# Optimization experiments

Hardware: AMD Instinct MI355X
Metric: run time of the kernel (lower is better)

## Reference

```python
import jax, jax.numpy as jnp
import numpy as np
from jax import lax

DN = ('NCDHW', 'OIDHW', 'NCDHW')
BN_EPS = 1e-5  # eval-mode BatchNorm3d with running_mean=0, running_var=1


def conv3d(x, w, b):
    y = lax.conv_general_dilated(x, w, window_strides=(1, 1, 1),
                                 padding=[(1, 1)] * 3, dimension_numbers=DN)
    return y + b[None, :, None, None, None]


def maxpool2(x):
    return lax.reduce_window(x, -jnp.inf, lax.max,
                             (1, 1, 2, 2, 2), (1, 1, 2, 2, 2), 'VALID')


def spline_block(x, cw, cb, knots, sw, w1, w2, g, beta):
    # SplineConv3d: conv -> (BSpline3D blend with SiLU) -> BN(eval) -> maxpool
    y = conv3d(x, cw, cb)                                   # [b,c,d,h,w]
    basis = jnp.maximum(y[..., None] - knots, 0.0) ** 3     # [b,c,d,h,w,k]
    sp = jnp.einsum('bcdhwk,ck->bcdhw', basis, sw)
    out = (w1[None, :, None, None, None] * sp
           + w2[None, :, None, None, None] * (y * jax.nn.sigmoid(y)))
    scale = (g / jnp.sqrt(1.0 + BN_EPS))[None, :, None, None, None]
    return maxpool2(out * scale + beta[None, :, None, None, None])


def setup_inputs() -> dict:
    key = jax.random.key(0)
    ks = iter(jax.random.split(key, 40))
    def nrm(shape, s=1.0):
        return jax.random.normal(next(ks), shape, dtype=jnp.float32) * s
    d = {}
    d['x'] = nrm((2, 1, 64, 64, 64))
    for cin, cout, t in [(1, 32, '1'), (32, 64, '2'), (64, 128, '3')]:
        d[f'c{t}_w'] = nrm((cout, cin, 3, 3, 3), 0.1)
        d[f'c{t}_b'] = nrm((cout,), 0.01)
        d[f'c{t}_knots'] = jnp.linspace(-1.0, 1.0, 10).astype(jnp.float32)
        d[f'c{t}_sw'] = nrm((cout, 10), 0.2)
        d[f'c{t}_w1'] = nrm((cout,), 0.2)
        d[f'c{t}_w2'] = nrm((cout,), 0.2)
        d[f'bn{t}_g'] = 1.0 + nrm((cout,), 0.1)
        d[f'bn{t}_b'] = nrm((cout,), 0.1)
    d['fc1_w'] = nrm((256, 128), 0.05)
    d['fc1_b'] = nrm((256,), 0.01)
    d['fc2_w'] = nrm((2, 256), 0.05)
    d['fc2_b'] = nrm((2,), 0.01)
    return d


def reference(x,
              c1_w, c1_b, c1_knots, c1_sw, c1_w1, c1_w2, bn1_g, bn1_b,
              c2_w, c2_b, c2_knots, c2_sw, c2_w1, c2_w2, bn2_g, bn2_b,
              c3_w, c3_b, c3_knots, c3_sw, c3_w1, c3_w2, bn3_g, bn3_b,
              fc1_w, fc1_b, fc2_w, fc2_b):
    h = spline_block(x, c1_w, c1_b, c1_knots, c1_sw, c1_w1, c1_w2, bn1_g, bn1_b)
    h = spline_block(h, c2_w, c2_b, c2_knots, c2_sw, c2_w1, c2_w2, bn2_g, bn2_b)
    h = spline_block(h, c3_w, c3_b, c3_knots, c3_sw, c3_w1, c3_w2, bn3_g, bn3_b)
    h = h.mean(axis=(2, 3, 4))          # AdaptiveAvgPool3d((1,1,1)) + flatten
    h = jax.nn.relu(h @ fc1_w.T + fc1_b)  # dropout is identity in eval mode
    return h @ fc2_w.T + fc2_b
```

## Files before the change

kernel.cpp:

```cpp
#include <hip/hip_runtime.h>
#include <math.h>


#define GLOBAL_AS __attribute__((address_space(1)))
#define LDS_AS    __attribute__((address_space(3)))

static __device__ __forceinline__ void async_ld16(const float* g, float* l) {
    __builtin_amdgcn_global_load_lds((const GLOBAL_AS void*)g, (LDS_AS void*)l,
                                     16, 0, 0);
}

__global__ __launch_bounds__(256) void repack_kernel(
    const float* __restrict__ w1, const float* __restrict__ w2,
    const float* __restrict__ w3,
    float* __restrict__ o1, float* __restrict__ o2, float* __restrict__ o3)
{
    const int i = blockIdx.x * 256 + threadIdx.x;
    const float* src;
    float* dst;
    if (i < 32)            { src = w1 + i * 27;           dst = o1 + i * 28; }
    else if (i < 2080)     { const int j = i - 32;   src = w2 + j * 27; dst = o2 + j * 28; }
    else if (i < 10272)    { const int j = i - 2080; src = w3 + j * 27; dst = o3 + j * 28; }
    else return;
#pragma unroll
    for (int t = 0; t < 27; t++) dst[t] = src[t];
    dst[27] = 0.0f;
}

template <int TPB_, int CIN, int CSPLIT, int G,
          int WDT, int WHT, int WWT, int BD, int BH, int BW>
__global__ __launch_bounds__(TPB_, 2) void spline_block_kernel(
    const float* __restrict__ x,
    const float4* __restrict__ wpk,
    const float* __restrict__ cb,
    const float* __restrict__ knots,
    const float* __restrict__ sw,
    const float* __restrict__ w1,
    const float* __restrict__ w2,
    const float* __restrict__ g,
    const float* __restrict__ beta,
    const float* __restrict__ zbuf,
    float* __restrict__ out,
    int N, int Cout, int D, int H, int W,
    int ntiles, int nthw, int ntw)
{
    constexpr int NSW    = BD * BH * BW;
    constexpr int NW     = TPB_ / 64;
    constexpr int CPG    = CIN / CSPLIT;
    constexpr int ID     = 2 * WDT + 2;
    constexpr int IH     = 2 * WHT + 2;
    constexpr int CHK    = (WWT + 4) / 2;
    constexpr int PITCH  = CHK * 4;
    constexpr int ROWS   = ID * IH;
    constexpr int CHUNKS = ROWS * CHK;
    constexpr int PHYS   = CHUNKS * 4;
    constexpr int NCH    = (CHUNKS + 63) / 64;
    constexpr int BUFS   = (CPG > 1) ? 2 : 1;
    static_assert(NW == NSW * CSPLIT, "waves = spatial-tiles x cin-split");
    static_assert(WDT * WHT * WWT == 64, "one wave per spatial tile");
    static_assert(CIN % CSPLIT == 0, "cin divisible");
    static_assert(NCH <= 32, "mask fits u32");
    static_assert(NCH == 6, "s_waitcnt vmcnt(6) literal assumes 6 issues/cin");
    static_assert(CSPLIT == 1 ||
                  (CSPLIT - 1) * 64 * G * 8 <= NW * BUFS * PHYS,
                  "reduction scratch fits in tile");

    __shared__ __align__(16) float tile[NW][BUFS][PHYS];
    __shared__ float4 stbl[G * 11];

    const int PD = D >> 1, PH = H >> 1, PW = W >> 1;
    const int groups = Cout / G;
    const int tid  = threadIdx.x;
    const int wv   = tid >> 6;
    const int lane = tid & 63;
    const int sw_  = wv % NSW;
    const int cg   = wv / NSW;

    const int bx      = blockIdx.x;
    const int tile_id = bx % ntiles;
    const int t1      = bx / ntiles;
    const int grp     = t1 % groups;
    const int n       = t1 / groups;
    const int c0      = grp * G;
    const int cinbase = cg * CPG;

    const int td  = tile_id / nthw;
    const int rem = tile_id % nthw;
    const int th_ = rem / ntw;
    const int tw_ = rem % ntw;

    for (int i = tid; i < G * 11; i += TPB_) {
        const int gg  = i / 11;
        const int cnt = i % 11;
        const int c   = c0 + gg;
        float A = 0.f, B3 = 0.f, C3 = 0.f, Dd = 0.f;
        for (int j = 0; j < cnt; j++) {
            const float s = sw[c * 10 + j];
            const float k = knots[j];
            A  += s;
            B3 += 3.0f * s * k;
            C3 += 3.0f * s * k * k;
            Dd += s * k * k * k;
        }
        stbl[i] = make_float4(A, B3, C3, Dd);
    }

    const int swd = sw_ / (BH * BW);
    const int r2  = sw_ % (BH * BW);
    const int swh = r2 / BW;
    const int sww = r2 % BW;
    const int pd0 = td  * (BD * WDT) + swd * WDT;
    const int ph0 = th_ * (BH * WHT) + swh * WHT;
    const int pw0 = tw_ * (BW * WWT) + sww * WWT;

    const int pwl = lane % WWT;
    const int phl = (lane / WWT) % WHT;
    const int pdl = lane / (WWT * WHT);

    const int d0 = 2 * pd0 - 1, h0 = 2 * ph0 - 1;
    const int w0 = 2 * pw0 - 1;
    const int wb = w0 & ~3;
    const int woff = w0 - wb;

    int off[NCH];
    unsigned vm = 0;
#pragma unroll
    for (int k = 0; k < NCH; k++) {
        const int chunk = lane + 64 * k;
        const int row = chunk / CHK, cs = chunk - row * CHK;
        const int dz = row / IH, hy = row - dz * IH;
        const int dd = d0 + dz, hh = h0 + hy;
        const int wsd = wb + cs * 4;
        const bool ok = (chunk < CHUNKS) &
                        ((unsigned)dd < (unsigned)D) &
                        ((unsigned)hh < (unsigned)H) &
                        ((unsigned)wsd < (unsigned)W);
        off[k] = ok ? (dd * H + hh) * W + wsd : 0;
        vm |= (unsigned)ok << k;
    }

    const size_t chstride = (size_t)D * H * W;
    const float* xn = x + (size_t)n * CIN * chstride;

    float acc[G][8];
#pragma unroll
    for (int gg = 0; gg < G; gg++)
#pragma unroll
        for (int i = 0; i < 8; i++) acc[gg][i] = 0.0f;

    __syncthreads();

    auto stage = [&](int ci, int buf) {
        const float* xc = xn + (size_t)ci * chstride;
        float* dst = &tile[wv][buf][0];
#pragma unroll
        for (int k = 0; k < NCH; k++) {
            const int chunk = lane + 64 * k;
            if ((k + 1) * 64 <= CHUNKS || chunk < CHUNKS) {
                const float* src = ((vm >> k) & 1) ? (xc + off[k]) : zbuf;
                async_ld16(src, dst + chunk * 4);
            }
        }
    };

    stage(cinbase, 0);

#pragma unroll 1
    for (int s = 0; s < CPG; s++) {
        const int cur = s & (BUFS - 1);
        if (s + 1 < CPG) {
            stage(cinbase + s + 1, cur ^ 1);
            asm volatile("s_waitcnt vmcnt(6)" ::: "memory");
        } else {
            asm volatile("s_waitcnt vmcnt(0)" ::: "memory");
        }

        const int ci = cinbase + s;
        const float* tb = &tile[wv][cur][0];
        float r[64];
#pragma unroll
        for (int dz = 0; dz < 4; dz++)
#pragma unroll
        for (int dy = 0; dy < 4; dy++) {
            const int rb = ((2 * pdl + dz) * IH + (2 * phl + dy)) * PITCH +
                           woff + 2 * pwl;
            r[(dz * 4 + dy) * 4 + 0] = tb[rb + 0];
            r[(dz * 4 + dy) * 4 + 1] = tb[rb + 1];
            r[(dz * 4 + dy) * 4 + 2] = tb[rb + 2];
            r[(dz * 4 + dy) * 4 + 3] = tb[rb + 3];
        }

#pragma unroll
        for (int gg = 0; gg < G; gg++) {
            const float4* wp = wpk + ((size_t)(c0 + gg) * CIN + ci) * 7;
            float4 q[7];
#pragma unroll
            for (int ch = 0; ch < 7; ch++) q[ch] = wp[ch];
#pragma unroll
            for (int ch = 0; ch < 7; ch++) {
#pragma unroll
                for (int j = 0; j < 4; j++) {
                    const int tap = ch * 4 + j;
                    if (tap < 27) {
                        const float wvj = (j == 0) ? q[ch].x : (j == 1) ? q[ch].y
                                        : (j == 2) ? q[ch].z : q[ch].w;
                        const int kd = tap / 9, kh = (tap % 9) / 3, kw = tap % 3;
#pragma unroll
                        for (int od = 0; od < 2; od++)
#pragma unroll
                        for (int oh = 0; oh < 2; oh++)
#pragma unroll
                        for (int ow = 0; ow < 2; ow++)
                            acc[gg][(od * 2 + oh) * 2 + ow] =
                                fmaf(wvj,
                                     r[((od + kd) * 4 + (oh + kh)) * 4 + (ow + kw)],
                                     acc[gg][(od * 2 + oh) * 2 + ow]);
                    }
                }
            }
        }
    }

    float* af = &acc[0][0];
    if (CSPLIT > 1) {
        __syncthreads();
        float* scratch = &tile[0][0][0];
        if (cg > 0) {
#pragma unroll
            for (int idx = 0; idx < G * 8; idx++)
                scratch[(idx * (CSPLIT - 1) + (cg - 1)) * 64 + lane] = af[idx];
        }
        __syncthreads();
        if (cg == 0) {
#pragma unroll
            for (int idx = 0; idx < G * 8; idx++) {
                float s2 = af[idx];
                for (int j = 0; j < CSPLIT - 1; j++)
                    s2 += scratch[(idx * (CSPLIT - 1) + j) * 64 + lane];
                af[idx] = s2;
            }
        }
    }

    if (cg == 0) {
        const int pdg = pd0 + pdl, phg = ph0 + phl, pwg = pw0 + pwl;
#pragma unroll
        for (int gg = 0; gg < G; gg++) {
            const int c = c0 + gg;
            const float bias = cb[c];
            const float W1 = w1[c], W2 = w2[c];
            const float scale = g[c] * rsqrtf(1.0f + 1e-5f);
            const float bb = beta[c];

            float m = -INFINITY;
#pragma unroll
            for (int i = 0; i < 8; i++) {
                const float y = acc[gg][i] + bias;
                int idx = (int)floorf((y + 1.0f) * 4.5f) + 1;
                idx = min(max(idx, 0), 10);
                const float4 cf = stbl[gg * 11 + idx];
                const float sp = ((cf.x * y - cf.y) * y + cf.z) * y - cf.w;
                const float silu = y / (1.0f + __expf(-y));
                const float o = fmaf(W1 * sp + W2 * silu, scale, bb);
                m = fmaxf(m, o);
            }
            out[((size_t)(n * Cout + c) * PD + pdg) * PH * PW + phg * PW + pwg] = m;
        }
    }
}

__global__ __launch_bounds__(64) void mean_kernel(
    const float* __restrict__ h, float* __restrict__ out, int S)
{
    const int nc = blockIdx.x;
    const int lane = threadIdx.x;
    const float* p = h + (size_t)nc * S;
    float s = 0.0f;
    for (int i = lane; i < S; i += 64) s += p[i];
#pragma unroll
    for (int off = 32; off > 0; off >>= 1) s += __shfl_down(s, off, 64);
    if (lane == 0) out[nc] = s / (float)S;
}

__global__ __launch_bounds__(256) void fc_kernel(
    const float* __restrict__ pooled,
    const float* __restrict__ w1, const float* __restrict__ b1,
    const float* __restrict__ w2, const float* __restrict__ b2,
    float* __restrict__ out)
{
    __shared__ float hbuf[2][256];
    const int j = threadIdx.x;
#pragma unroll
    for (int nn = 0; nn < 2; nn++) {
        float s = b1[j];
        for (int k = 0; k < 128; k++)
            s = fmaf(pooled[nn * 128 + k], w1[j * 128 + k], s);
        hbuf[nn][j] = fmaxf(s, 0.0f);
    }
    __syncthreads();
    const int wid = j >> 6, lane = j & 63;
    const int nn = wid >> 1, oo = wid & 1;
    float s = 0.0f;
    for (int k = lane; k < 256; k += 64) s += hbuf[nn][k] * w2[oo * 256 + k];
#pragma unroll
    for (int off = 32; off > 0; off >>= 1) s += __shfl_down(s, off, 64);
    if (lane == 0) out[nn * 2 + oo] = s + b2[oo];
}

extern "C" void kernel_launch(void* const* d_in, const int* in_sizes, int n_in,
                              void* d_out, int out_size, void* d_ws, size_t ws_size,
                              hipStream_t stream) {
    const float* x      = (const float*)d_in[0];
    const float* c1_w   = (const float*)d_in[1];
    const float* c1_b   = (const float*)d_in[2];
    const float* c1_kn  = (const float*)d_in[3];
    const float* c1_sw  = (const float*)d_in[4];
    const float* c1_w1  = (const float*)d_in[5];
    const float* c1_w2  = (const float*)d_in[6];
    const float* bn1_g  = (const float*)d_in[7];
    const float* bn1_b  = (const float*)d_in[8];
    const float* c2_w   = (const float*)d_in[9];
    const float* c2_b   = (const float*)d_in[10];
    const float* c2_kn  = (const float*)d_in[11];
    const float* c2_sw  = (const float*)d_in[12];
    const float* c2_w1  = (const float*)d_in[13];
    const float* c2_w2  = (const float*)d_in[14];
    const float* bn2_g  = (const float*)d_in[15];
    const float* bn2_b  = (const float*)d_in[16];
    const float* c3_w   = (const float*)d_in[17];
    const float* c3_b   = (const float*)d_in[18];
    const float* c3_kn  = (const float*)d_in[19];
    const float* c3_sw  = (const float*)d_in[20];
    const float* c3_w1  = (const float*)d_in[21];
    const float* c3_w2  = (const float*)d_in[22];
    const float* bn3_g  = (const float*)d_in[23];
    const float* bn3_b  = (const float*)d_in[24];
    const float* fc1_w  = (const float*)d_in[25];
    const float* fc1_b  = (const float*)d_in[26];
    const float* fc2_w  = (const float*)d_in[27];
    const float* fc2_b  = (const float*)d_in[28];

    float* ws = (float*)d_ws;
    float* h1     = ws;
    float* h2     = h1 + 2097152;
    float* h3     = h2 + 524288;
    float* pooled = h3 + 131072;
    float* zbuf   = pooled + 256;
    float* wp1    = zbuf + 16;
    float* wp2    = wp1 + 896;
    float* wp3    = wp2 + 57344;

    hipMemsetAsync(zbuf, 0, 64, stream);

    repack_kernel<<<dim3(41), dim3(256), 0, stream>>>(c1_w, c2_w, c3_w,
                                                      wp1, wp2, wp3);

    spline_block_kernel<256, 1, 1, 4, 2, 4, 8, 2, 2, 1>
        <<<dim3(2048), dim3(256), 0, stream>>>(
        x, (const float4*)wp1, c1_b, c1_kn, c1_sw, c1_w1, c1_w2, bn1_g, bn1_b,
        zbuf, h1, 2, 32, 64, 64, 64, 128, 16, 4);
    spline_block_kernel<256, 32, 2, 4, 2, 4, 8, 1, 1, 2>
        <<<dim3(1024), dim3(256), 0, stream>>>(
        h1, (const float4*)wp2, c2_b, c2_kn, c2_sw, c2_w1, c2_w2, bn2_g, bn2_b,
        zbuf, h2, 2, 64, 32, 32, 32, 32, 4, 1);
    spline_block_kernel<256, 64, 4, 4, 2, 4, 8, 1, 1, 1>
        <<<dim3(512), dim3(256), 0, stream>>>(
        h2, (const float4*)wp3, c3_b, c3_kn, c3_sw, c3_w1, c3_w2, bn3_g, bn3_b,
        zbuf, h3, 2, 128, 16, 16, 16, 8, 2, 1);
    mean_kernel<<<dim3(256), dim3(64), 0, stream>>>(h3, pooled, 512);
    fc_kernel<<<dim3(1), dim3(256), 0, stream>>>(pooled, fc1_w, fc1_b, fc2_w, fc2_b,
                                                 (float*)d_out);
}
```

Measured before the change: 327.8 us.

## Replace double-buffered LDS DMA with register-staged single-buffer prefetch

For layers with multiple input channels per wave, the async global-to-LDS double buffer is replaced by a single LDS tile per wave. The next channel's inputs are loaded into registers in two halves, overlapped with the current channel's LDS reads and FMA loop, and written into LDS after each half of the work. This halves LDS use, which may allow more blocks per CU, at the cost of extra VGPRs and explicit ds_write instructions. It also makes the weight index wave-uniform via readfirstlane, fixes the cross-wave reduction scratch indexing for multiple spatial sub-tiles, and folds the zero-buffer memset into the repack kernel.

```diff
diff --git a/kernel.cpp b/kernel.cpp
--- a/kernel.cpp
+++ b/kernel.cpp
@@ -13,7 +13,8 @@
 __global__ __launch_bounds__(256) void repack_kernel(
     const float* __restrict__ w1, const float* __restrict__ w2,
     const float* __restrict__ w3,
-    float* __restrict__ o1, float* __restrict__ o2, float* __restrict__ o3)
+    float* __restrict__ o1, float* __restrict__ o2, float* __restrict__ o3,
+    float* __restrict__ zbuf)
 {
     const int i = blockIdx.x * 256 + threadIdx.x;
     const float* src;
@@ -21,7 +22,7 @@
     if (i < 32)            { src = w1 + i * 27;           dst = o1 + i * 28; }
     else if (i < 2080)     { const int j = i - 32;   src = w2 + j * 27; dst = o2 + j * 28; }
     else if (i < 10272)    { const int j = i - 2080; src = w3 + j * 27; dst = o3 + j * 28; }
-    else return;
+    else { if (i < 10288) zbuf[i - 10272] = 0.0f; return; }
 #pragma unroll
     for (int t = 0; t < 27; t++) dst[t] = src[t];
     dst[27] = 0.0f;
@@ -55,17 +56,16 @@
     constexpr int CHUNKS = ROWS * CHK;
     constexpr int PHYS   = CHUNKS * 4;
     constexpr int NCH    = (CHUNKS + 63) / 64;
-    constexpr int BUFS   = (CPG > 1) ? 2 : 1;
+    constexpr int SCRDW  = (CSPLIT > 1) ? (CSPLIT - 1) * NSW * 64 * G * 8 : 0;
+    constexpr int TILEDW = (NW * PHYS > SCRDW) ? NW * PHYS : SCRDW;
     static_assert(NW == NSW * CSPLIT, "waves = spatial-tiles x cin-split");
     static_assert(WDT * WHT * WWT == 64, "one wave per spatial tile");
     static_assert(CIN % CSPLIT == 0, "cin divisible");
+    static_assert(G == 4, "acc layout assumes G==4");
     static_assert(NCH <= 32, "mask fits u32");
-    static_assert(NCH == 6, "s_waitcnt vmcnt(6) literal assumes 6 issues/cin");
-    static_assert(CSPLIT == 1 ||
-                  (CSPLIT - 1) * 64 * G * 8 <= NW * BUFS * PHYS,
-                  "reduction scratch fits in tile");
-
-    __shared__ __align__(16) float tile[NW][BUFS][PHYS];
+    static_assert(CPG == 1 || NCH == 6, "reg-staged A/B split assumes 6 chunks");
+
+    __shared__ __align__(16) float tile[TILEDW];
     __shared__ float4 stbl[G * 11];
 
     const int PD = D >> 1, PH = H >> 1, PW = W >> 1;
@@ -83,6 +83,7 @@
     const int n       = t1 / groups;
     const int c0      = grp * G;
     const int cinbase = cg * CPG;
+    const int cinbase_u = __builtin_amdgcn_readfirstlane(cinbase);
 
     const int td  = tile_id / nthw;
     const int rem = tile_id % nthw;
@@ -141,6 +142,7 @@
 
     const size_t chstride = (size_t)D * H * W;
     const float* xn = x + (size_t)n * CIN * chstride;
+    float* myt = tile + wv * PHYS;
 
     float acc[G][8];
 #pragma unroll
@@ -150,33 +152,63 @@
 
     __syncthreads();
 
-    auto stage = [&](int ci, int buf) {
+    auto stage_dma = [&](int ci) {
         const float* xc = xn + (size_t)ci * chstride;
-        float* dst = &tile[wv][buf][0];
 #pragma unroll
         for (int k = 0; k < NCH; k++) {
             const int chunk = lane + 64 * k;
             if ((k + 1) * 64 <= CHUNKS || chunk < CHUNKS) {
                 const float* src = ((vm >> k) & 1) ? (xc + off[k]) : zbuf;
-                async_ld16(src, dst + chunk * 4);
+                async_ld16(src, myt + chunk * 4);
             }
         }
     };
-
-    stage(cinbase, 0);
+    float4 nxa[3], nxb[3];
+    auto ld_a = [&](int ci) {
+        const float* xc = xn + (size_t)ci * chstride;
+#pragma unroll
+        for (int k = 0; k < 3; k++) {
+            const float* src = ((vm >> k) & 1) ? (xc + off[k]) : zbuf;
+            nxa[k] = *reinterpret_cast<const float4*>(src);
+        }
+    };
+    auto ld_b = [&](int ci) {
+        const float* xc = xn + (size_t)ci * chstride;
+#pragma unroll
+        for (int k = 3; k < NCH; k++) {
+            const float* src = ((vm >> k) & 1) ? (xc + off[k]) : zbuf;
+            nxb[k - 3] = *reinterpret_cast<const float4*>(src);
+        }
+    };
+    auto wr_a = [&]() {
+#pragma unroll
+        for (int k = 0; k < 3; k++)
+            *reinterpret_cast<float4*>(myt + (lane + 64 * k) * 4) = nxa[k];
+    };
+    auto wr_b = [&]() {
+#pragma unroll
+        for (int k = 3; k < NCH; k++) {
+            const int chunk = lane + 64 * k;
+            if ((k + 1) * 64 <= CHUNKS || chunk < CHUNKS)
+                *reinterpret_cast<float4*>(myt + chunk * 4) = nxb[k - 3];
+        }
+    };
+
+    if constexpr (CPG == 1) {
+        stage_dma(cinbase);
+        asm volatile("s_waitcnt vmcnt(0)" ::: "memory");
+    } else {
+        ld_a(cinbase); wr_a();
+        ld_b(cinbase); wr_b();
+    }
 
 #pragma unroll 1
     for (int s = 0; s < CPG; s++) {
-        const int cur = s & (BUFS - 1);
-        if (s + 1 < CPG) {
-            stage(cinbase + s + 1, cur ^ 1);
-            asm volatile("s_waitcnt vmcnt(6)" ::: "memory");
-        } else {
-            asm volatile("s_waitcnt vmcnt(0)" ::: "memory");
-        }
-
-        const int ci = cinbase + s;
-        const float* tb = &tile[wv][cur][0];
+        if constexpr (CPG > 1) {
+            if (s + 1 < CPG) ld_a(cinbase + s + 1);
+        }
+
+        const int ci_u = cinbase_u + s;
         float r[64];
 #pragma unroll
         for (int dz = 0; dz < 4; dz++)
@@ -184,18 +216,25 @@
         for (int dy = 0; dy < 4; dy++) {
             const int rb = ((2 * pdl + dz) * IH + (2 * phl + dy)) * PITCH +
                            woff + 2 * pwl;
-            r[(dz * 4 + dy) * 4 + 0] = tb[rb + 0];
-            r[(dz * 4 + dy) * 4 + 1] = tb[rb + 1];
-            r[(dz * 4 + dy) * 4 + 2] = tb[rb + 2];
-            r[(dz * 4 + dy) * 4 + 3] = tb[rb + 3];
+            r[(dz * 4 + dy) * 4 + 0] = myt[rb + 0];
+            r[(dz * 4 + dy) * 4 + 1] = myt[rb + 1];
+            r[(dz * 4 + dy) * 4 + 2] = myt[rb + 2];
+            r[(dz * 4 + dy) * 4 + 3] = myt[rb + 3];
+        }
+
+        if constexpr (CPG > 1) {
+            if (s + 1 < CPG) {
+                wr_a();
+                ld_b(cinbase + s + 1);
+            }
         }
 
 #pragma unroll
         for (int gg = 0; gg < G; gg++) {
-            const float4* wp = wpk + ((size_t)(c0 + gg) * CIN + ci) * 7;
+            const float4* wq = wpk + ((size_t)(c0 + gg) * CIN + ci_u) * 7;
             float4 q[7];
 #pragma unroll
-            for (int ch = 0; ch < 7; ch++) q[ch] = wp[ch];
+            for (int ch = 0; ch < 7; ch++) q[ch] = wq[ch];
 #pragma unroll
             for (int ch = 0; ch < 7; ch++) {
 #pragma unroll
@@ -219,16 +258,21 @@
                 }
             }
         }
+
+        if constexpr (CPG > 1) {
+            if (s + 1 < CPG) wr_b();
+        }
     }
 
     float* af = &acc[0][0];
     if (CSPLIT > 1) {
         __syncthreads();
-        float* scratch = &tile[0][0][0];
+        float* scratch = tile;
         if (cg > 0) {
 #pragma unroll
             for (int idx = 0; idx < G * 8; idx++)
-                scratch[(idx * (CSPLIT - 1) + (cg - 1)) * 64 + lane] = af[idx];
+                scratch[((idx * (CSPLIT - 1) + (cg - 1)) * NSW + sw_) * 64 + lane]
+                    = af[idx];
         }
         __syncthreads();
         if (cg == 0) {
@@ -236,7 +280,7 @@
             for (int idx = 0; idx < G * 8; idx++) {
                 float s2 = af[idx];
                 for (int j = 0; j < CSPLIT - 1; j++)
-                    s2 += scratch[(idx * (CSPLIT - 1) + j) * 64 + lane];
+                    s2 += scratch[((idx * (CSPLIT - 1) + j) * NSW + sw_) * 64 + lane];
                 af[idx] = s2;
             }
         }
@@ -251,7 +295,6 @@
             const float W1 = w1[c], W2 = w2[c];
             const float scale = g[c] * rsqrtf(1.0f + 1e-5f);
             const float bb = beta[c];
-
             float m = -INFINITY;
 #pragma unroll
             for (int i = 0; i < 8; i++) {
@@ -350,10 +393,8 @@
     float* wp2    = wp1 + 896;
     float* wp3    = wp2 + 57344;
 
-    hipMemsetAsync(zbuf, 0, 64, stream);
-
     repack_kernel<<<dim3(41), dim3(256), 0, stream>>>(c1_w, c2_w, c3_w,
-                                                      wp1, wp2, wp3);
+                                                      wp1, wp2, wp3, zbuf);
 
     spline_block_kernel<256, 1, 1, 4, 2, 4, 8, 2, 2, 1>
         <<<dim3(2048), dim3(256), 0, stream>>>(
```

After: 388.4 us. 1.18x slower.

## Fuse global mean into last spline block via atomics, fold memset into repack

Applied to the files above, without the earlier changes.

The third spline block now reduces its pooled outputs per wave and atomically adds the scaled sums into the pooled buffer, which removes the separate mean kernel and the h3 round trip. The zbuf memset is folded into the repack kernel, which also zeroes the pooled buffer. The cin-split reduction scratch indexing is now per spatial wave, and the cin base is made wave-uniform with readfirstlane so weight loads can become scalar. Atomics make the summation order nondeterministic.

```diff
diff --git a/kernel.cpp b/kernel.cpp
--- a/kernel.cpp
+++ b/kernel.cpp
@@ -13,7 +13,8 @@
 __global__ __launch_bounds__(256) void repack_kernel(
     const float* __restrict__ w1, const float* __restrict__ w2,
     const float* __restrict__ w3,
-    float* __restrict__ o1, float* __restrict__ o2, float* __restrict__ o3)
+    float* __restrict__ o1, float* __restrict__ o2, float* __restrict__ o3,
+    float* __restrict__ zbuf, float* __restrict__ pooled)
 {
     const int i = blockIdx.x * 256 + threadIdx.x;
     const float* src;
@@ -21,14 +22,18 @@
     if (i < 32)            { src = w1 + i * 27;           dst = o1 + i * 28; }
     else if (i < 2080)     { const int j = i - 32;   src = w2 + j * 27; dst = o2 + j * 28; }
     else if (i < 10272)    { const int j = i - 2080; src = w3 + j * 27; dst = o3 + j * 28; }
-    else return;
+    else {
+        if (i < 10288) zbuf[i - 10272] = 0.0f;
+        else if (i < 10544) pooled[i - 10288] = 0.0f;
+        return;
+    }
 #pragma unroll
     for (int t = 0; t < 27; t++) dst[t] = src[t];
     dst[27] = 0.0f;
 }
 
 template <int TPB_, int CIN, int CSPLIT, int G,
-          int WDT, int WHT, int WWT, int BD, int BH, int BW>
+          int WDT, int WHT, int WWT, int BD, int BH, int BW, bool FMEAN>
 __global__ __launch_bounds__(TPB_, 2) void spline_block_kernel(
     const float* __restrict__ x,
     const float4* __restrict__ wpk,
@@ -59,10 +64,11 @@
     static_assert(NW == NSW * CSPLIT, "waves = spatial-tiles x cin-split");
     static_assert(WDT * WHT * WWT == 64, "one wave per spatial tile");
     static_assert(CIN % CSPLIT == 0, "cin divisible");
+    static_assert(G == 4, "acc layout assumes G==4");
     static_assert(NCH <= 32, "mask fits u32");
     static_assert(NCH == 6, "s_waitcnt vmcnt(6) literal assumes 6 issues/cin");
     static_assert(CSPLIT == 1 ||
-                  (CSPLIT - 1) * 64 * G * 8 <= NW * BUFS * PHYS,
+                  (CSPLIT - 1) * NSW * 64 * G * 8 <= NW * BUFS * PHYS,
                   "reduction scratch fits in tile");
 
     __shared__ __align__(16) float tile[NW][BUFS][PHYS];
@@ -83,6 +89,7 @@
     const int n       = t1 / groups;
     const int c0      = grp * G;
     const int cinbase = cg * CPG;
+    const int cinbase_u = __builtin_amdgcn_readfirstlane(cinbase);
 
     const int td  = tile_id / nthw;
     const int rem = tile_id % nthw;
@@ -175,7 +182,7 @@
             asm volatile("s_waitcnt vmcnt(0)" ::: "memory");
         }
 
-        const int ci = cinbase + s;
+        const int ci_u = cinbase_u + s;
         const float* tb = &tile[wv][cur][0];
         float r[64];
 #pragma unroll
@@ -192,10 +199,10 @@
 
 #pragma unroll
         for (int gg = 0; gg < G; gg++) {
-            const float4* wp = wpk + ((size_t)(c0 + gg) * CIN + ci) * 7;
+            const float4* wq = wpk + ((size_t)(c0 + gg) * CIN + ci_u) * 7;
             float4 q[7];
 #pragma unroll
-            for (int ch = 0; ch < 7; ch++) q[ch] = wp[ch];
+            for (int ch = 0; ch < 7; ch++) q[ch] = wq[ch];
 #pragma unroll
             for (int ch = 0; ch < 7; ch++) {
 #pragma unroll
@@ -228,7 +235,8 @@
         if (cg > 0) {
 #pragma unroll
             for (int idx = 0; idx < G * 8; idx++)
-                scratch[(idx * (CSPLIT - 1) + (cg - 1)) * 64 + lane] = af[idx];
+                scratch[((idx * (CSPLIT - 1) + (cg - 1)) * NSW + sw_) * 64 + lane]
+                    = af[idx];
         }
         __syncthreads();
         if (cg == 0) {
@@ -236,7 +244,7 @@
             for (int idx = 0; idx < G * 8; idx++) {
                 float s2 = af[idx];
                 for (int j = 0; j < CSPLIT - 1; j++)
-                    s2 += scratch[(idx * (CSPLIT - 1) + j) * 64 + lane];
+                    s2 += scratch[((idx * (CSPLIT - 1) + j) * NSW + sw_) * 64 + lane];
                 af[idx] = s2;
             }
         }
@@ -244,6 +252,7 @@
 
     if (cg == 0) {
         const int pdg = pd0 + pdl, phg = ph0 + phl, pwg = pw0 + pwl;
+        const float inv_vol = 1.0f / (float)(PD * PH * PW);
 #pragma unroll
         for (int gg = 0; gg < G; gg++) {
             const int c = c0 + gg;
@@ -251,7 +260,6 @@
             const float W1 = w1[c], W2 = w2[c];
             const float scale = g[c] * rsqrtf(1.0f + 1e-5f);
             const float bb = beta[c];
-
             float m = -INFINITY;
 #pragma unroll
             for (int i = 0; i < 8; i++) {
@@ -264,22 +272,19 @@
                 const float o = fmaf(W1 * sp + W2 * silu, scale, bb);
                 m = fmaxf(m, o);
             }
-            out[((size_t)(n * Cout + c) * PD + pdg) * PH * PW + phg * PW + pwg] = m;
-        }
-    }
-}
-
-__global__ __launch_bounds__(64) void mean_kernel(
-    const float* __restrict__ h, float* __restrict__ out, int S)
-{
-    const int nc = blockIdx.x;
-    const int lane = threadIdx.x;
-    const float* p = h + (size_t)nc * S;
-    float s = 0.0f;
-    for (int i = lane; i < S; i += 64) s += p[i];
-#pragma unroll
-    for (int off = 32; off > 0; off >>= 1) s += __shfl_down(s, off, 64);
-    if (lane == 0) out[nc] = s / (float)S;
+            if constexpr (FMEAN) {
+                float ssum = m;
+#pragma unroll
+                for (int o2 = 32; o2 > 0; o2 >>= 1)
+                    ssum += __shfl_down(ssum, o2, 64);
+                if (lane == 0)
+                    atomicAdd(&out[(size_t)n * Cout + c], ssum * inv_vol);
+            } else {
+                out[((size_t)(n * Cout + c) * PD + pdg) * PH * PW +
+                    phg * PW + pwg] = m;
+            }
+        }
+    }
 }
 
 __global__ __launch_bounds__(256) void fc_kernel(
@@ -343,31 +348,27 @@
     float* ws = (float*)d_ws;
     float* h1     = ws;
     float* h2     = h1 + 2097152;
-    float* h3     = h2 + 524288;
-    float* pooled = h3 + 131072;
+    float* pooled = h2 + 524288;
     float* zbuf   = pooled + 256;
     float* wp1    = zbuf + 16;
     float* wp2    = wp1 + 896;
     float* wp3    = wp2 + 57344;
 
-    hipMemsetAsync(zbuf, 0, 64, stream);
-
-    repack_kernel<<<dim3(41), dim3(256), 0, stream>>>(c1_w, c2_w, c3_w,
-                                                      wp1, wp2, wp3);
-
-    spline_block_kernel<256, 1, 1, 4, 2, 4, 8, 2, 2, 1>
+    repack_kernel<<<dim3(42), dim3(256), 0, stream>>>(c1_w, c2_w, c3_w,
+                                                      wp1, wp2, wp3, zbuf, pooled);
+
+    spline_block_kernel<256, 1, 1, 4, 2, 4, 8, 2, 2, 1, false>
         <<<dim3(2048), dim3(256), 0, stream>>>(
         x, (const float4*)wp1, c1_b, c1_kn, c1_sw, c1_w1, c1_w2, bn1_g, bn1_b,
         zbuf, h1, 2, 32, 64, 64, 64, 128, 16, 4);
-    spline_block_kernel<256, 32, 2, 4, 2, 4, 8, 1, 1, 2>
+    spline_block_kernel<256, 32, 2, 4, 2, 4, 8, 1, 1, 2, false>
         <<<dim3(1024), dim3(256), 0, stream>>>(
         h1, (const float4*)wp2, c2_b, c2_kn, c2_sw, c2_w1, c2_w2, bn2_g, bn2_b,
         zbuf, h2, 2, 64, 32, 32, 32, 32, 4, 1);
-    spline_block_kernel<256, 64, 4, 4, 2, 4, 8, 1, 1, 1>
+    spline_block_kernel<256, 64, 4, 4, 2, 4, 8, 1, 1, 1, true>
         <<<dim3(512), dim3(256), 0, stream>>>(
         h2, (const float4*)wp3, c3_b, c3_kn, c3_sw, c3_w1, c3_w2, bn3_g, bn3_b,
-        zbuf, h3, 2, 128, 16, 16, 16, 8, 2, 1);
-    mean_kernel<<<dim3(256), dim3(64), 0, stream>>>(h3, pooled, 512);
+        zbuf, pooled, 2, 128, 16, 16, 16, 8, 2, 1);
     fc_kernel<<<dim3(1), dim3(256), 0, stream>>>(pooled, fc1_w, fc1_b, fc2_w, fc2_b,
                                                  (float*)d_out);
 }
```

After: 320.6 us. 1.02x faster.
